# Optimization experiments

Hardware: AMD Instinct MI355X
Metric: run time of the kernel (lower is better)

## Reference

```python
import jax, jax.numpy as jnp
import numpy as np

NUM_HEADS = 16
EMBED_DIM = 1024
HEAD_DIM = EMBED_DIM // NUM_HEADS


def setup_inputs() -> dict:
    key = jax.random.key(0)
    ks = jax.random.split(key, 9)
    B, S, D = 4, 2048, EMBED_DIM
    scale = 1.0 / np.sqrt(D)
    inp = {
        "x": jax.random.normal(ks[0], (B, S, D), dtype=jnp.float32),
        "Wq": jax.random.normal(ks[1], (D, D), dtype=jnp.float32) * scale,
        "bq": jnp.zeros((D,), dtype=jnp.float32),
        "Wk": jax.random.normal(ks[2], (D, D), dtype=jnp.float32) * scale,
        "bk": jnp.zeros((D,), dtype=jnp.float32),
        "Wv": jax.random.normal(ks[3], (D, D), dtype=jnp.float32) * scale,
        "bv": jnp.zeros((D,), dtype=jnp.float32),
        "Wo": jax.random.normal(ks[4], (D, D), dtype=jnp.float32) * scale,
        "bo": jnp.zeros((D,), dtype=jnp.float32),
    }
    return inp


def reference(x, Wq, bq, Wk, bk, Wv, bv, Wo, bo):
    # x: [B, S, D]; weights stored torch-style as [out, in] -> use x @ W.T + b
    B, S, D = x.shape
    H, Hd = NUM_HEADS, HEAD_DIM

    def proj(W, b):
        return (jnp.einsum('bsd,ed->bse', x, W) + b).reshape(B, S, H, Hd).transpose(0, 2, 1, 3)

    Q = proj(Wq, bq)  # [B, H, S, Hd]
    K = proj(Wk, bk)
    V = proj(Wv, bv)

    scores = jnp.einsum('bhqd,bhkd->bhqk', Q, K) / jnp.sqrt(jnp.float32(Hd))
    attn = jax.nn.softmax(scores, axis=-1)  # dropout is identity in eval mode
    context = jnp.einsum('bhqk,bhkd->bhqd', attn, V)
    context = context.transpose(0, 2, 1, 3).reshape(B, S, D)
    out = jnp.einsum('bsd,ed->bse', context, Wo) + bo
    return out
```

## Files before the change

### kernel.cpp

```cpp
#include <hip/hip_runtime.h>


#define LOG2E 1.4426950408889634f
#define QSCALE (0.125f * LOG2E)

typedef __bf16 bf16x8 __attribute__((ext_vector_type(8)));
typedef float f32x4 __attribute__((ext_vector_type(4)));
typedef unsigned short u16x4 __attribute__((ext_vector_type(4)));
typedef unsigned short u16x8 __attribute__((ext_vector_type(8)));
typedef unsigned int u32x4 __attribute__((ext_vector_type(4)));

__device__ __forceinline__ unsigned short f2bf(float f) {
  unsigned int u = __builtin_bit_cast(unsigned int, f);
  u += 0x7fffu + ((u >> 16) & 1u);
  return (unsigned short)(u >> 16);
}

__device__ __forceinline__ unsigned int pack2bf(float a, float b) {
  unsigned int ua = __builtin_bit_cast(unsigned int, a);
  unsigned int ub = __builtin_bit_cast(unsigned int, b);
  ua += 0x7fffu + ((ua >> 16) & 1u);
  ub += 0x7fffu + ((ub >> 16) & 1u);
  return __builtin_amdgcn_perm(ub, ua, 0x07060302u);
}

typedef const __attribute__((address_space(1))) void* gptr_t;
typedef __attribute__((address_space(3))) void* lptr_t;
__device__ __forceinline__ void gload16(const void* g, void* l) {
  __builtin_amdgcn_global_load_lds((gptr_t)g, (lptr_t)l, 16, 0, 0);
}

__global__ __launch_bounds__(256) void k_cvt_x(const float* __restrict__ x,
                                               unsigned short* __restrict__ xb) {
  int i = (blockIdx.x * 256 + threadIdx.x) * 4;
  f32x4 v = *(const f32x4*)(x + i);
  u16x4 o; o[0] = f2bf(v[0]); o[1] = f2bf(v[1]); o[2] = f2bf(v[2]); o[3] = f2bf(v[3]);
  *(u16x4*)(xb + i) = o;
}

__global__ __launch_bounds__(256) void k_cvt_w(const float* __restrict__ Wq, const float* __restrict__ Wk,
                                               const float* __restrict__ Wv, const float* __restrict__ Wo,
                                               unsigned short* __restrict__ Wb) {
  int i = (blockIdx.x * 256 + threadIdx.x) * 4;
  int wsel = i >> 20;
  int loc = i & 1048575;
  const float* src = (wsel == 0) ? Wq : (wsel == 1) ? Wk : (wsel == 2) ? Wv : Wo;
  float sc = (wsel == 0) ? QSCALE : 1.0f;
  f32x4 v = *(const f32x4*)(src + loc);
  u16x4 o; o[0] = f2bf(v[0] * sc); o[1] = f2bf(v[1] * sc); o[2] = f2bf(v[2] * sc); o[3] = f2bf(v[3] * sc);
  *(u16x4*)(Wb + i) = o;
}

__global__ __launch_bounds__(256, 2) void k_gemm_qkv(
    const unsigned short* __restrict__ xb, const unsigned short* __restrict__ Wb,
    const float* __restrict__ bq, const float* __restrict__ bk, const float* __restrict__ bv,
    unsigned short* __restrict__ Qb, unsigned short* __restrict__ Kb, unsigned short* __restrict__ Vtb) {
  __shared__ unsigned short As[128 * 32];
  __shared__ unsigned short Bs[128 * 32];
  const int tid = threadIdx.x;
  const int lane = tid & 63;
  const int w = tid >> 6;
  const int wm = w & 1;
  const int wn = w >> 1;
  const int z = blockIdx.z;
  const int m0 = blockIdx.y * 128;
  const int n0 = blockIdx.x * 128;
  const unsigned short* W = Wb + ((size_t)z << 20);

  const int srow = tid >> 2;
  const int sch = (tid & 3) << 3;
  const size_t a0 = (size_t)(m0 + srow) * 1024 + sch;
  const size_t b0 = (size_t)(n0 + srow) * 1024 + sch;

  f32x4 zero4 = {0.f, 0.f, 0.f, 0.f};
  f32x4 acc[4][4];
#pragma unroll
  for (int i = 0; i < 4; ++i)
#pragma unroll
    for (int jj = 0; jj < 4; ++jj) acc[i][jj] = zero4;

  const int fr = lane & 15;
  const int fk = (lane >> 4) << 3;

  for (int kt = 0; kt < 32; ++kt) {
    const int ko = kt << 5;
    __syncthreads();
    gload16(xb + a0 + ko, As + tid * 8);
    gload16(xb + a0 + (size_t)65536 + ko, As + 2048 + tid * 8);
    gload16(W + b0 + ko, Bs + tid * 8);
    gload16(W + b0 + (size_t)65536 + ko, Bs + 2048 + tid * 8);
    __syncthreads();
    bf16x8 af[4], bfr[4];
#pragma unroll
    for (int mt = 0; mt < 4; ++mt)
      af[mt] = *(const bf16x8*)&As[(wm * 64 + mt * 16 + fr) * 32 + fk];
#pragma unroll
    for (int nt = 0; nt < 4; ++nt)
      bfr[nt] = *(const bf16x8*)&Bs[(wn * 64 + nt * 16 + fr) * 32 + fk];
#pragma unroll
    for (int mt = 0; mt < 4; ++mt)
#pragma unroll
      for (int nt = 0; nt < 4; ++nt)
        acc[mt][nt] = __builtin_amdgcn_mfma_f32_16x16x32_bf16(af[mt], bfr[nt], acc[mt][nt], 0, 0, 0);
  }

  const float* bias = (z == 0) ? bq : (z == 1) ? bk : bv;
  const float bsc = (z == 0) ? QSCALE : 1.0f;
  const int rg = (lane >> 4) << 2;
#pragma unroll
  for (int mt = 0; mt < 4; ++mt) {
    const int mb = m0 + wm * 64 + mt * 16 + rg;
    const int b = mb >> 11;
    const int s = mb & 2047;
#pragma unroll
    for (int nt = 0; nt < 4; ++nt) {
      const int n = n0 + wn * 64 + nt * 16 + fr;
      const float bvv = bias[n] * bsc;
      const int h = n >> 6;
      const int d = n & 63;
      if (z == 2) {
        u16x4 pk;
#pragma unroll
        for (int r = 0; r < 4; ++r) pk[r] = f2bf(acc[mt][nt][r] + bvv);
        const int pbase = (s & ~31) | ((s & 12) << 1) | ((s & 16) >> 2);
        *(u16x4*)&Vtb[(((size_t)(b * 16 + h) << 6) + d) * 2048 + pbase] = pk;
      } else {
        unsigned short* O = (z == 0) ? Qb : Kb;
#pragma unroll
        for (int r = 0; r < 4; ++r)
          O[(((size_t)(b * 16 + h) << 11) + s + r) * 64 + d] = f2bf(acc[mt][nt][r] + bvv);
      }
    }
  }
}

__global__ __launch_bounds__(256, 3) void k_flash(
    const unsigned short* __restrict__ Qb, const unsigned short* __restrict__ Kb,
    const unsigned short* __restrict__ Vtb, unsigned short* __restrict__ Ctx) {
  __shared__ unsigned short Ks[128 * 64];
  __shared__ unsigned short Vts[64 * 128];
  const int tid = threadIdx.x;
  const int lane = tid & 63;
  const int wq = tid >> 6;
  const int fr = lane & 15;
  const int qd = lane >> 4;
  const int bh = blockIdx.y;
  const int q0 = blockIdx.x << 7;
  const size_t hoff = (size_t)bh << 17;
  const unsigned short* Qh = Qb + hoff + ((size_t)q0 << 6);
  const unsigned short* Kh = Kb + hoff;
  const unsigned short* Vh = Vtb + hoff;

  bf16x8 qf[2][2];
#pragma unroll
  for (int qt = 0; qt < 2; ++qt)
#pragma unroll
    for (int ds = 0; ds < 2; ++ds)
      qf[qt][ds] = *(const bf16x8*)&Qh[(wq * 32 + qt * 16 + fr) * 64 + ds * 32 + qd * 8];

  f32x4 zero4 = {0.f, 0.f, 0.f, 0.f};
  f32x4 o_acc[2][4];
  float l_p[2] = {0.f, 0.f};
#pragma unroll
  for (int mt = 0; mt < 2; ++mt)
#pragma unroll
    for (int dt = 0; dt < 4; ++dt) o_acc[mt][dt] = zero4;

  for (int j = 0; j < 16; ++j) {
    const int k0 = j << 7;
    __syncthreads();
#pragma unroll
    for (int p = 0; p < 4; ++p) {
      int slot = p * 256 + tid;
      int kr = slot >> 3;
      int ch = slot & 7;
      gload16(Kh + (size_t)(k0 + kr) * 64 + ((ch ^ (kr & 7)) << 3), Ks + slot * 8);
    }
#pragma unroll
    for (int p = 0; p < 4; ++p) {
      int slot = p * 256 + tid;
      int dr = slot >> 4;
      int ch = slot & 15;
      gload16(Vh + (size_t)dr * 2048 + k0 + ((ch ^ (dr & 15)) << 3), Vts + slot * 8);
    }
    __syncthreads();

    f32x4 st[2][8];
#pragma unroll
    for (int qt = 0; qt < 2; ++qt)
#pragma unroll
      for (int kt = 0; kt < 8; ++kt) st[qt][kt] = zero4;
#pragma unroll
    for (int kt = 0; kt < 8; ++kt) {
#pragma unroll
      for (int ds = 0; ds < 2; ++ds) {
        int key = kt * 16 + fr;
        int c = ds * 4 + qd;
        bf16x8 kf = *(const bf16x8*)&Ks[key * 64 + ((c ^ (key & 7)) << 3)];
#pragma unroll
        for (int qt = 0; qt < 2; ++qt)
          st[qt][kt] = __builtin_amdgcn_mfma_f32_16x16x32_bf16(kf, qf[qt][ds], st[qt][kt], 0, 0, 0);
      }
    }

#pragma unroll
    for (int qt = 0; qt < 2; ++qt) {
      float ps0 = 0.f, ps1 = 0.f;
#pragma unroll
      for (int kt = 0; kt < 8; ++kt) {
#pragma unroll
        for (int r = 0; r < 4; ++r) st[qt][kt][r] = __builtin_amdgcn_exp2f(st[qt][kt][r]);
        ps0 += st[qt][kt][0] + st[qt][kt][2];
        ps1 += st[qt][kt][1] + st[qt][kt][3];
      }
      l_p[qt] += ps0 + ps1;
    }

#pragma unroll
    for (int ks = 0; ks < 4; ++ks) {
      bf16x8 pf[2];
#pragma unroll
      for (int mt = 0; mt < 2; ++mt) {
        u32x4 pk;
        pk[0] = pack2bf(st[mt][2 * ks][0], st[mt][2 * ks][1]);
        pk[1] = pack2bf(st[mt][2 * ks][2], st[mt][2 * ks][3]);
        pk[2] = pack2bf(st[mt][2 * ks + 1][0], st[mt][2 * ks + 1][1]);
        pk[3] = pack2bf(st[mt][2 * ks + 1][2], st[mt][2 * ks + 1][3]);
        pf[mt] = __builtin_bit_cast(bf16x8, pk);
      }
#pragma unroll
      for (int dt = 0; dt < 4; ++dt) {
        int d = dt * 16 + fr;
        int c = ks * 4 + qd;
        bf16x8 vf = *(const bf16x8*)&Vts[d * 128 + ((c ^ (d & 15)) << 3)];
#pragma unroll
        for (int mt = 0; mt < 2; ++mt)
          o_acc[mt][dt] = __builtin_amdgcn_mfma_f32_16x16x32_bf16(pf[mt], vf, o_acc[mt][dt], 0, 0, 0);
      }
    }
  }

  float l_red[2];
#pragma unroll
  for (int mt = 0; mt < 2; ++mt) {
    float lv = l_p[mt];
    lv += __shfl_xor(lv, 16);
    lv += __shfl_xor(lv, 32);
    l_red[mt] = lv;
  }

  const int b = bh >> 4;
  const int h = bh & 15;
#pragma unroll
  for (int mt = 0; mt < 2; ++mt) {
#pragma unroll
    for (int r = 0; r < 4; ++r) {
      float lv = __shfl(l_red[mt], qd * 4 + r);
      float rl = 1.0f / lv;
      int s = q0 + wq * 32 + mt * 16 + qd * 4 + r;
      size_t base = (((size_t)b * 2048 + s) << 10) + (h << 6);
#pragma unroll
      for (int dt = 0; dt < 4; ++dt) Ctx[base + dt * 16 + fr] = f2bf(o_acc[mt][dt][r] * rl);
    }
  }
}

__global__ __launch_bounds__(256, 2) void k_gemm_out(
    const unsigned short* __restrict__ Ctx, const unsigned short* __restrict__ Wo,
    const float* __restrict__ bo, float* __restrict__ out) {
  __shared__ unsigned short As[128 * 32];
  __shared__ unsigned short Bs[128 * 32];
  const int tid = threadIdx.x;
  const int lane = tid & 63;
  const int w = tid >> 6;
  const int wm = w & 1;
  const int wn = w >> 1;
  const int m0 = blockIdx.y * 128;
  const int n0 = blockIdx.x * 128;

  const int srow = tid >> 2;
  const int sch = (tid & 3) << 3;
  const size_t a0 = (size_t)(m0 + srow) * 1024 + sch;
  const size_t b0 = (size_t)(n0 + srow) * 1024 + sch;

  f32x4 zero4 = {0.f, 0.f, 0.f, 0.f};
  f32x4 acc[4][4];
#pragma unroll
  for (int i = 0; i < 4; ++i)
#pragma unroll
    for (int jj = 0; jj < 4; ++jj) acc[i][jj] = zero4;

  const int fr = lane & 15;
  const int fk = (lane >> 4) << 3;

  for (int kt = 0; kt < 32; ++kt) {
    const int ko = kt << 5;
    __syncthreads();
    gload16(Ctx + a0 + ko, As + tid * 8);
    gload16(Ctx + a0 + (size_t)65536 + ko, As + 2048 + tid * 8);
    gload16(Wo + b0 + ko, Bs + tid * 8);
    gload16(Wo + b0 + (size_t)65536 + ko, Bs + 2048 + tid * 8);
    __syncthreads();
    bf16x8 af[4], bfr[4];
#pragma unroll
    for (int mt = 0; mt < 4; ++mt)
      af[mt] = *(const bf16x8*)&As[(wm * 64 + mt * 16 + fr) * 32 + fk];
#pragma unroll
    for (int nt = 0; nt < 4; ++nt)
      bfr[nt] = *(const bf16x8*)&Bs[(wn * 64 + nt * 16 + fr) * 32 + fk];
#pragma unroll
    for (int mt = 0; mt < 4; ++mt)
#pragma unroll
      for (int nt = 0; nt < 4; ++nt)
        acc[mt][nt] = __builtin_amdgcn_mfma_f32_16x16x32_bf16(af[mt], bfr[nt], acc[mt][nt], 0, 0, 0);
  }

  const int rg = (lane >> 4) << 2;
#pragma unroll
  for (int mt = 0; mt < 4; ++mt) {
    const int mb = m0 + wm * 64 + mt * 16 + rg;
#pragma unroll
    for (int nt = 0; nt < 4; ++nt) {
      const int n = n0 + wn * 64 + nt * 16 + fr;
      const float bvv = bo[n];
#pragma unroll
      for (int r = 0; r < 4; ++r)
        out[(size_t)(mb + r) * 1024 + n] = acc[mt][nt][r] + bvv;
    }
  }
}

extern "C" void kernel_launch(void* const* d_in, const int* in_sizes, int n_in,
                              void* d_out, int out_size, void* d_ws, size_t ws_size,
                              hipStream_t stream) {
  (void)in_sizes; (void)n_in; (void)out_size; (void)ws_size;
  const float* x = (const float*)d_in[0];
  const float* Wq = (const float*)d_in[1];
  const float* bq = (const float*)d_in[2];
  const float* Wk = (const float*)d_in[3];
  const float* bk = (const float*)d_in[4];
  const float* Wv = (const float*)d_in[5];
  const float* bv = (const float*)d_in[6];
  const float* Wo = (const float*)d_in[7];
  const float* bo = (const float*)d_in[8];
  float* out = (float*)d_out;

  unsigned short* xb = (unsigned short*)d_ws;
  unsigned short* Wb = xb + 8388608;
  unsigned short* Qb = Wb + 4194304;
  unsigned short* Kb = Qb + 8388608;
  unsigned short* Vtb = Kb + 8388608;
  unsigned short* Ctx = xb;

  k_cvt_x<<<8192, 256, 0, stream>>>(x, xb);
  k_cvt_w<<<4096, 256, 0, stream>>>(Wq, Wk, Wv, Wo, Wb);
  k_gemm_qkv<<<dim3(8, 64, 3), 256, 0, stream>>>(xb, Wb, bq, bk, bv, Qb, Kb, Vtb);
  k_flash<<<dim3(16, 64), 256, 0, stream>>>(Qb, Kb, Vtb, Ctx);
  k_gemm_out<<<dim3(8, 64), 256, 0, stream>>>(Ctx, Wb + 3 * 1048576, bo, out);
}
```

Measured before the change: 292.1 us.

## Double flash query tile per block and merge conversion kernels into one launch

```diff
diff --git a/kernel.cpp b/kernel.cpp
--- a/kernel.cpp
+++ b/kernel.cpp
@@ -30,25 +30,25 @@
   __builtin_amdgcn_global_load_lds((gptr_t)g, (lptr_t)l, 16, 0, 0);
 }
 
-__global__ __launch_bounds__(256) void k_cvt_x(const float* __restrict__ x,
-                                               unsigned short* __restrict__ xb) {
-  int i = (blockIdx.x * 256 + threadIdx.x) * 4;
-  f32x4 v = *(const f32x4*)(x + i);
-  u16x4 o; o[0] = f2bf(v[0]); o[1] = f2bf(v[1]); o[2] = f2bf(v[2]); o[3] = f2bf(v[3]);
-  *(u16x4*)(xb + i) = o;
-}
-
-__global__ __launch_bounds__(256) void k_cvt_w(const float* __restrict__ Wq, const float* __restrict__ Wk,
-                                               const float* __restrict__ Wv, const float* __restrict__ Wo,
-                                               unsigned short* __restrict__ Wb) {
-  int i = (blockIdx.x * 256 + threadIdx.x) * 4;
-  int wsel = i >> 20;
-  int loc = i & 1048575;
-  const float* src = (wsel == 0) ? Wq : (wsel == 1) ? Wk : (wsel == 2) ? Wv : Wo;
-  float sc = (wsel == 0) ? QSCALE : 1.0f;
-  f32x4 v = *(const f32x4*)(src + loc);
-  u16x4 o; o[0] = f2bf(v[0] * sc); o[1] = f2bf(v[1] * sc); o[2] = f2bf(v[2] * sc); o[3] = f2bf(v[3] * sc);
-  *(u16x4*)(Wb + i) = o;
+__global__ __launch_bounds__(256) void k_cvt(const float* __restrict__ x,
+                                             const float* __restrict__ Wq, const float* __restrict__ Wk,
+                                             const float* __restrict__ Wv, const float* __restrict__ Wo,
+                                             unsigned short* __restrict__ xb, unsigned short* __restrict__ Wb) {
+  int gi = (blockIdx.x * 256 + threadIdx.x) * 4;
+  if (gi < 8388608) {
+    f32x4 v = *(const f32x4*)(x + gi);
+    u16x4 o; o[0] = f2bf(v[0]); o[1] = f2bf(v[1]); o[2] = f2bf(v[2]); o[3] = f2bf(v[3]);
+    *(u16x4*)(xb + gi) = o;
+  } else {
+    int i = gi - 8388608;
+    int wsel = i >> 20;
+    int loc = i & 1048575;
+    const float* src = (wsel == 0) ? Wq : (wsel == 1) ? Wk : (wsel == 2) ? Wv : Wo;
+    float sc = (wsel == 0) ? QSCALE : 1.0f;
+    f32x4 v = *(const f32x4*)(src + loc);
+    u16x4 o; o[0] = f2bf(v[0] * sc); o[1] = f2bf(v[1] * sc); o[2] = f2bf(v[2] * sc); o[3] = f2bf(v[3] * sc);
+    *(u16x4*)(Wb + i) = o;
+  }
 }
 
 __global__ __launch_bounds__(256, 2) void k_gemm_qkv(
@@ -134,7 +134,7 @@
   }
 }
 
-__global__ __launch_bounds__(256, 3) void k_flash(
+__global__ __launch_bounds__(256, 2) void k_flash(
     const unsigned short* __restrict__ Qb, const unsigned short* __restrict__ Kb,
     const unsigned short* __restrict__ Vtb, unsigned short* __restrict__ Ctx) {
   __shared__ unsigned short Ks[128 * 64];
@@ -145,26 +145,26 @@
   const int fr = lane & 15;
   const int qd = lane >> 4;
   const int bh = blockIdx.y;
-  const int q0 = blockIdx.x << 7;
+  const int q0 = blockIdx.x << 8;
   const size_t hoff = (size_t)bh << 17;
   const unsigned short* Qh = Qb + hoff + ((size_t)q0 << 6);
   const unsigned short* Kh = Kb + hoff;
   const unsigned short* Vh = Vtb + hoff;
 
-  bf16x8 qf[2][2];
-#pragma unroll
-  for (int qt = 0; qt < 2; ++qt)
+  bf16x8 qf[4][2];
+#pragma unroll
+  for (int qt = 0; qt < 4; ++qt)
 #pragma unroll
     for (int ds = 0; ds < 2; ++ds)
-      qf[qt][ds] = *(const bf16x8*)&Qh[(wq * 32 + qt * 16 + fr) * 64 + ds * 32 + qd * 8];
+      qf[qt][ds] = *(const bf16x8*)&Qh[(wq * 64 + qt * 16 + fr) * 64 + ds * 32 + qd * 8];
 
   f32x4 zero4 = {0.f, 0.f, 0.f, 0.f};
-  f32x4 o_acc[2][4];
-  float l_p[2] = {0.f, 0.f};
-#pragma unroll
-  for (int mt = 0; mt < 2; ++mt)
-#pragma unroll
-    for (int dt = 0; dt < 4; ++dt) o_acc[mt][dt] = zero4;
+  f32x4 o_acc[4][4];
+  float l_p[4] = {0.f, 0.f, 0.f, 0.f};
+#pragma unroll
+  for (int qt = 0; qt < 4; ++qt)
+#pragma unroll
+    for (int dt = 0; dt < 4; ++dt) o_acc[qt][dt] = zero4;
 
   for (int j = 0; j < 16; ++j) {
     const int k0 = j << 7;
@@ -185,48 +185,54 @@
     }
     __syncthreads();
 
-    f32x4 st[2][8];
-#pragma unroll
-    for (int qt = 0; qt < 2; ++qt)
-#pragma unroll
-      for (int kt = 0; kt < 8; ++kt) st[qt][kt] = zero4;
-#pragma unroll
-    for (int kt = 0; kt < 8; ++kt) {
-#pragma unroll
-      for (int ds = 0; ds < 2; ++ds) {
-        int key = kt * 16 + fr;
-        int c = ds * 4 + qd;
-        bf16x8 kf = *(const bf16x8*)&Ks[key * 64 + ((c ^ (key & 7)) << 3)];
-#pragma unroll
-        for (int qt = 0; qt < 2; ++qt)
-          st[qt][kt] = __builtin_amdgcn_mfma_f32_16x16x32_bf16(kf, qf[qt][ds], st[qt][kt], 0, 0, 0);
-      }
-    }
-
-#pragma unroll
-    for (int qt = 0; qt < 2; ++qt) {
-      float ps0 = 0.f, ps1 = 0.f;
+    unsigned int ppk[4][8][2];
+
+#pragma unroll
+    for (int pr = 0; pr < 2; ++pr) {
+      f32x4 st[2][8];
+#pragma unroll
+      for (int q2 = 0; q2 < 2; ++q2)
+#pragma unroll
+        for (int kt = 0; kt < 8; ++kt) st[q2][kt] = zero4;
 #pragma unroll
       for (int kt = 0; kt < 8; ++kt) {
 #pragma unroll
-        for (int r = 0; r < 4; ++r) st[qt][kt][r] = __builtin_amdgcn_exp2f(st[qt][kt][r]);
-        ps0 += st[qt][kt][0] + st[qt][kt][2];
-        ps1 += st[qt][kt][1] + st[qt][kt][3];
-      }
-      l_p[qt] += ps0 + ps1;
+        for (int ds = 0; ds < 2; ++ds) {
+          int key = kt * 16 + fr;
+          int c = ds * 4 + qd;
+          bf16x8 kf = *(const bf16x8*)&Ks[key * 64 + ((c ^ (key & 7)) << 3)];
+          st[0][kt] = __builtin_amdgcn_mfma_f32_16x16x32_bf16(kf, qf[2 * pr][ds], st[0][kt], 0, 0, 0);
+          st[1][kt] = __builtin_amdgcn_mfma_f32_16x16x32_bf16(kf, qf[2 * pr + 1][ds], st[1][kt], 0, 0, 0);
+        }
+      }
+#pragma unroll
+      for (int q2 = 0; q2 < 2; ++q2) {
+        const int qt = 2 * pr + q2;
+        float ps0 = 0.f, ps1 = 0.f;
+#pragma unroll
+        for (int kt = 0; kt < 8; ++kt) {
+#pragma unroll
+          for (int r = 0; r < 4; ++r) st[q2][kt][r] = __builtin_amdgcn_exp2f(st[q2][kt][r]);
+          ps0 += st[q2][kt][0] + st[q2][kt][2];
+          ps1 += st[q2][kt][1] + st[q2][kt][3];
+          ppk[qt][kt][0] = pack2bf(st[q2][kt][0], st[q2][kt][1]);
+          ppk[qt][kt][1] = pack2bf(st[q2][kt][2], st[q2][kt][3]);
+        }
+        l_p[qt] += ps0 + ps1;
+      }
     }
 
 #pragma unroll
     for (int ks = 0; ks < 4; ++ks) {
-      bf16x8 pf[2];
-#pragma unroll
-      for (int mt = 0; mt < 2; ++mt) {
+      bf16x8 pf[4];
+#pragma unroll
+      for (int qt = 0; qt < 4; ++qt) {
         u32x4 pk;
-        pk[0] = pack2bf(st[mt][2 * ks][0], st[mt][2 * ks][1]);
-        pk[1] = pack2bf(st[mt][2 * ks][2], st[mt][2 * ks][3]);
-        pk[2] = pack2bf(st[mt][2 * ks + 1][0], st[mt][2 * ks + 1][1]);
-        pk[3] = pack2bf(st[mt][2 * ks + 1][2], st[mt][2 * ks + 1][3]);
-        pf[mt] = __builtin_bit_cast(bf16x8, pk);
+        pk[0] = ppk[qt][2 * ks][0];
+        pk[1] = ppk[qt][2 * ks][1];
+        pk[2] = ppk[qt][2 * ks + 1][0];
+        pk[3] = ppk[qt][2 * ks + 1][1];
+        pf[qt] = __builtin_bit_cast(bf16x8, pk);
       }
 #pragma unroll
       for (int dt = 0; dt < 4; ++dt) {
@@ -234,33 +240,33 @@
         int c = ks * 4 + qd;
         bf16x8 vf = *(const bf16x8*)&Vts[d * 128 + ((c ^ (d & 15)) << 3)];
 #pragma unroll
-        for (int mt = 0; mt < 2; ++mt)
-          o_acc[mt][dt] = __builtin_amdgcn_mfma_f32_16x16x32_bf16(pf[mt], vf, o_acc[mt][dt], 0, 0, 0);
-      }
-    }
-  }
-
-  float l_red[2];
-#pragma unroll
-  for (int mt = 0; mt < 2; ++mt) {
-    float lv = l_p[mt];
+        for (int qt = 0; qt < 4; ++qt)
+          o_acc[qt][dt] = __builtin_amdgcn_mfma_f32_16x16x32_bf16(pf[qt], vf, o_acc[qt][dt], 0, 0, 0);
+      }
+    }
+  }
+
+  float l_red[4];
+#pragma unroll
+  for (int qt = 0; qt < 4; ++qt) {
+    float lv = l_p[qt];
     lv += __shfl_xor(lv, 16);
     lv += __shfl_xor(lv, 32);
-    l_red[mt] = lv;
+    l_red[qt] = lv;
   }
 
   const int b = bh >> 4;
   const int h = bh & 15;
 #pragma unroll
-  for (int mt = 0; mt < 2; ++mt) {
+  for (int qt = 0; qt < 4; ++qt) {
 #pragma unroll
     for (int r = 0; r < 4; ++r) {
-      float lv = __shfl(l_red[mt], qd * 4 + r);
+      float lv = __shfl(l_red[qt], qd * 4 + r);
       float rl = 1.0f / lv;
-      int s = q0 + wq * 32 + mt * 16 + qd * 4 + r;
+      int s = q0 + wq * 64 + qt * 16 + qd * 4 + r;
       size_t base = (((size_t)b * 2048 + s) << 10) + (h << 6);
 #pragma unroll
-      for (int dt = 0; dt < 4; ++dt) Ctx[base + dt * 16 + fr] = f2bf(o_acc[mt][dt][r] * rl);
+      for (int dt = 0; dt < 4; ++dt) Ctx[base + dt * 16 + fr] = f2bf(o_acc[qt][dt][r] * rl);
     }
   }
 }
@@ -352,9 +358,8 @@
   unsigned short* Vtb = Kb + 8388608;
   unsigned short* Ctx = xb;
 
-  k_cvt_x<<<8192, 256, 0, stream>>>(x, xb);
-  k_cvt_w<<<4096, 256, 0, stream>>>(Wq, Wk, Wv, Wo, Wb);
+  k_cvt<<<12288, 256, 0, stream>>>(x, Wq, Wk, Wv, Wo, xb, Wb);
   k_gemm_qkv<<<dim3(8, 64, 3), 256, 0, stream>>>(xb, Wb, bq, bk, bv, Qb, Kb, Vtb);
-  k_flash<<<dim3(16, 64), 256, 0, stream>>>(Qb, Kb, Vtb, Ctx);
+  k_flash<<<dim3(8, 64), 256, 0, stream>>>(Qb, Kb, Vtb, Ctx);
   k_gemm_out<<<dim3(8, 64), 256, 0, stream>>>(Ctx, Wb + 3 * 1048576, bo, out);
 }
```

Result: slower. 314.8 us (+7.8%).
